# Kernel optimization log

Measured on AMD Instinct MI355X. Metric: run time of the kernel, lower is better.

The kernel has to match this reference:

```python
import jax, jax.numpy as jnp
import numpy as np
import math

B, T, O, D, H, L, FF = 2, 1024, 512, 1024, 16, 4, 4096
MAX_SEQ = 1024


def _ln(x, g, b, eps=1e-5):
    m = jnp.mean(x, -1, keepdims=True)
    v = jnp.mean((x - m) ** 2, -1, keepdims=True)
    return (x - m) * jax.lax.rsqrt(v + eps) * g + b


def _gelu(x):
    return jax.nn.gelu(x, approximate=False)  # torch nn.GELU default = exact erf


def setup_inputs() -> dict:
    key = jax.random.key(0)
    ks = iter(jax.random.split(key, 64))
    std = 0.02
    def w(shape):
        return (jax.random.normal(next(ks), shape, jnp.float32) * std)
    d = {
        'obs': jax.random.normal(next(ks), (B, T, O), jnp.float32),
        # encoder MLP: Linear(O,D), LN, GELU, Linear(D,D), GELU, Linear(D,D), LN
        'enc_w1': w((O, D)), 'enc_b1': jnp.zeros((D,)),
        'enc_g1': jnp.ones((D,)), 'enc_be1': jnp.zeros((D,)),
        'enc_w2': w((D, D)), 'enc_b2': jnp.zeros((D,)),
        'enc_w3': w((D, D)), 'enc_b3': jnp.zeros((D,)),
        'enc_g2': jnp.ones((D,)), 'enc_be2': jnp.zeros((D,)),
        'pos_emb': w((MAX_SEQ, D)),
        # stacked per-layer transformer params [L, ...]
        'ln1_g': jnp.ones((L, D)), 'ln1_b': jnp.zeros((L, D)),
        'wq': w((L, D, D)), 'bq': jnp.zeros((L, D)),
        'wk': w((L, D, D)), 'bk': jnp.zeros((L, D)),
        'wv': w((L, D, D)), 'bv': jnp.zeros((L, D)),
        'wo': w((L, D, D)), 'bo': jnp.zeros((L, D)),
        'ln2_g': jnp.ones((L, D)), 'ln2_b': jnp.zeros((L, D)),
        'mlp_w1': w((L, D, FF)), 'mlp_b1': jnp.zeros((L, FF)),
        'mlp_w2': w((L, FF, D)), 'mlp_b2': jnp.zeros((L, D)),
        'lnf_g': jnp.ones((D,)), 'lnf_b': jnp.zeros((D,)),
        'dec_w': w((D, O)), 'dec_b': jnp.zeros((O,)),
    }
    return d


def reference(obs, enc_w1, enc_b1, enc_g1, enc_be1, enc_w2, enc_b2, enc_w3, enc_b3,
              enc_g2, enc_be2, pos_emb, ln1_g, ln1_b, wq, bq, wk, bk, wv, bv, wo, bo,
              ln2_g, ln2_b, mlp_w1, mlp_b1, mlp_w2, mlp_b2, lnf_g, lnf_b, dec_w, dec_b):
    b, t, _ = obs.shape
    dh = D // H
    scale = 1.0 / math.sqrt(dh)
    # embedder MLP
    h = _gelu(_ln(obs @ enc_w1 + enc_b1, enc_g1, enc_be1))
    h = _gelu(h @ enc_w2 + enc_b2)
    h = _ln(h @ enc_w3 + enc_b3, enc_g2, enc_be2)
    x = h + pos_emb[:t]
    # causal mask [t, t]
    mask = jnp.tril(jnp.ones((t, t), bool))

    def block(x, p):
        g1, b1, Wq, Bq, Wk, Bk, Wv, Bv, Wo, Bo, g2, b2, W1, B1, W2, B2 = p
        hn = _ln(x, g1, b1)
        q = (hn @ Wq + Bq).reshape(b, t, H, dh).transpose(0, 2, 1, 3)
        k = (hn @ Wk + Bk).reshape(b, t, H, dh).transpose(0, 2, 1, 3)
        v = (hn @ Wv + Bv).reshape(b, t, H, dh).transpose(0, 2, 1, 3)
        att = jnp.einsum('bhtd,bhsd->bhts', q, k) * scale
        att = jnp.where(mask, att, -jnp.inf)
        att = jax.nn.softmax(att, axis=-1)
        y = jnp.einsum('bhts,bhsd->bhtd', att, v)
        y = y.transpose(0, 2, 1, 3).reshape(b, t, D)
        x = x + y @ Wo + Bo
        hm = _ln(x, g2, b2)
        x = x + _gelu(hm @ W1 + B1) @ W2 + B2
        return x, None

    stacked = (ln1_g, ln1_b, wq, bq, wk, bk, wv, bv, wo, bo,
               ln2_g, ln2_b, mlp_w1, mlp_b1, mlp_w2, mlp_b2)
    x, _ = jax.lax.scan(block, x, stacked)
    x = _ln(x, lnf_g, lnf_b)
    out_obs = x @ dec_w + dec_b
    return x, out_obs
```

## Files before the change

### kernel.cpp

```cpp
#include <hip/hip_runtime.h>
#include <utility>

typedef unsigned short u16;
typedef __bf16  bf16x8 __attribute__((ext_vector_type(8)));
typedef float   f32x4  __attribute__((ext_vector_type(4)));
typedef unsigned short u16x4 __attribute__((ext_vector_type(4)));

constexpr int Bc = 2, Tc = 1024, Oc = 512, Dc = 1024, Hc = 16, Lc = 4, FFc = 4096;
constexpr int Mc = Bc * Tc;
constexpr int Sq = 3 * Dc;

__device__ __forceinline__ u16 f2b(float f) {
    unsigned u = __float_as_uint(f);
    u = (u + 0x7fffu + ((u >> 16) & 1u)) >> 16;
    return (u16)u;
}
__device__ __forceinline__ float gelu_f(float x) {
    return 0.5f * x * (1.0f + erff(x * 0.7071067811865476f));
}

typedef const __attribute__((address_space(1))) void* gas_p;
typedef __attribute__((address_space(3))) void* las_p;
__device__ __forceinline__ void gload16(const void* g, void* l) {
    __builtin_amdgcn_global_load_lds((gas_p)g, (las_p)l, 16, 0, 0);
}

__global__ __launch_bounds__(256) void wtrans(const float* __restrict__ in,
                                              u16* __restrict__ out, int R, int C,
                                              long inBatch, long outBatch) {
    __shared__ float t[32][33];
    const float* inp = in + (size_t)blockIdx.z * inBatch;
    u16* outp = out + (size_t)blockIdx.z * outBatch;
    const int tx = threadIdx.x & 31, ty = threadIdx.x >> 5;
    const int br = blockIdx.y * 32, bc = blockIdx.x * 32;
#pragma unroll
    for (int i = 0; i < 32; i += 8)
        t[ty + i][tx] = inp[(size_t)(br + ty + i) * C + bc + tx];
    __syncthreads();
#pragma unroll
    for (int i = 0; i < 32; i += 8)
        outp[(size_t)(bc + ty + i) * R + br + tx] = f2b(t[tx][ty + i]);
}

__global__ __launch_bounds__(256) void cvt_bf(const float* __restrict__ in,
                                              u16* __restrict__ out, int n) {
    int i = blockIdx.x * 256 + threadIdx.x;
    if (i * 4 >= n) return;
    float4 v = ((const float4*)in)[i];
    u16x4 r;
    r[0] = f2b(v.x); r[1] = f2b(v.y); r[2] = f2b(v.z); r[3] = f2b(v.w);
    ((u16x4*)out)[i] = r;
}

__global__ __launch_bounds__(256) void pack_qkv_bias(const float* __restrict__ bq,
    const float* __restrict__ bk, const float* __restrict__ bv, float* __restrict__ out) {
    int i = blockIdx.x * 256 + threadIdx.x;
    int l = i / Sq, j = i % Sq;
    float v = (j < Dc) ? bq[l * Dc + j] : (j < 2 * Dc ? bk[l * Dc + j - Dc] : bv[l * Dc + j - 2 * Dc]);
    out[i] = v;
}

__global__ __launch_bounds__(256) void ln_kernel(
    const float* __restrict__ in, const float* __restrict__ gam,
    const float* __restrict__ bet, const float* __restrict__ pos,
    float* __restrict__ outf, u16* __restrict__ outb, int do_gelu) {
    const int row = blockIdx.x, tid = threadIdx.x;
    const float4 v = ((const float4*)(in + (size_t)row * Dc))[tid];
    float s  = v.x + v.y + v.z + v.w;
    float ss = v.x * v.x + v.y * v.y + v.z * v.z + v.w * v.w;
#pragma unroll
    for (int m = 1; m < 64; m <<= 1) {
        s  += __shfl_xor(s,  m, 64);
        ss += __shfl_xor(ss, m, 64);
    }
    __shared__ float red[8];
    const int w = tid >> 6;
    if ((tid & 63) == 0) { red[w] = s; red[4 + w] = ss; }
    __syncthreads();
    s  = red[0] + red[1] + red[2] + red[3];
    ss = red[4] + red[5] + red[6] + red[7];
    const float mean = s * (1.0f / Dc);
    const float rstd = rsqrtf(ss * (1.0f / Dc) - mean * mean + 1e-5f);
    const float4 gv = ((const float4*)gam)[tid];
    const float4 bv = ((const float4*)bet)[tid];
    float y0 = (v.x - mean) * rstd * gv.x + bv.x;
    float y1 = (v.y - mean) * rstd * gv.y + bv.y;
    float y2 = (v.z - mean) * rstd * gv.z + bv.z;
    float y3 = (v.w - mean) * rstd * gv.w + bv.w;
    if (do_gelu) { y0 = gelu_f(y0); y1 = gelu_f(y1); y2 = gelu_f(y2); y3 = gelu_f(y3); }
    if (pos) {
        const float4 pv = ((const float4*)(pos + (size_t)(row & (Tc - 1)) * Dc))[tid];
        y0 += pv.x; y1 += pv.y; y2 += pv.z; y3 += pv.w;
    }
    if (outf) {
        float4 o; o.x = y0; o.y = y1; o.z = y2; o.w = y3;
        ((float4*)(outf + (size_t)row * Dc))[tid] = o;
    }
    if (outb) {
        u16x4 r; r[0] = f2b(y0); r[1] = f2b(y1); r[2] = f2b(y2); r[3] = f2b(y3);
        ((u16x4*)(outb + (size_t)row * Dc))[tid] = r;
    }
}

__global__ __launch_bounds__(256) void red2_ln(
    const float* __restrict__ p, const float* __restrict__ bias,
    const float* __restrict__ resid, float* __restrict__ xfout,
    const float* __restrict__ gam, const float* __restrict__ bet,
    float* __restrict__ lnoutf, u16* __restrict__ lnoutb) {
    const int row = blockIdx.x, tid = threadIdx.x;
    const f32x4 a  = ((const f32x4*)(p + (size_t)row * Dc))[tid];
    const f32x4 b  = ((const f32x4*)(p + (size_t)Mc * Dc + (size_t)row * Dc))[tid];
    const f32x4 bb = ((const f32x4*)bias)[tid];
    const f32x4 r  = ((const f32x4*)(resid + (size_t)row * Dc))[tid];
    f32x4 v;
#pragma unroll
    for (int j = 0; j < 4; ++j) v[j] = a[j] + b[j] + bb[j] + r[j];
    ((f32x4*)(xfout + (size_t)row * Dc))[tid] = v;
    float s  = v[0] + v[1] + v[2] + v[3];
    float ss = v[0]*v[0] + v[1]*v[1] + v[2]*v[2] + v[3]*v[3];
#pragma unroll
    for (int m = 1; m < 64; m <<= 1) {
        s  += __shfl_xor(s,  m, 64);
        ss += __shfl_xor(ss, m, 64);
    }
    __shared__ float red[8];
    const int w = tid >> 6;
    if ((tid & 63) == 0) { red[w] = s; red[4 + w] = ss; }
    __syncthreads();
    s  = red[0] + red[1] + red[2] + red[3];
    ss = red[4] + red[5] + red[6] + red[7];
    const float mean = s * (1.0f / Dc);
    const float rstd = rsqrtf(ss * (1.0f / Dc) - mean * mean + 1e-5f);
    const f32x4 gv = ((const f32x4*)gam)[tid];
    const f32x4 bv = ((const f32x4*)bet)[tid];
    f32x4 y;
#pragma unroll
    for (int j = 0; j < 4; ++j) y[j] = (v[j] - mean) * rstd * gv[j] + bv[j];
    if (lnoutf) ((f32x4*)(lnoutf + (size_t)row * Dc))[tid] = y;
    u16x4 o;
#pragma unroll
    for (int j = 0; j < 4; ++j) o[j] = f2b(y[j]);
    ((u16x4*)(lnoutb + (size_t)row * Dc))[tid] = o;
}

template<int BM, int BN, int FM, int FN, int WM, int WN, int OCC>
__global__ __launch_bounds__(256, OCC) void gemm_k(
    const u16* __restrict__ A, const u16* __restrict__ Bt,
    const float* __restrict__ bias, const float* resid,
    float* Cf, u16* Cb, u16* vTout, int vcol0,
    int M, int N, int Kst, int Kl, int do_gelu) {
    __shared__ u16 sA[2][BM][64];
    __shared__ u16 sB[2][BN][64];
    constexpr int NA = BM / 32;
    constexpr int NB = BN / 32;
    const int tid = threadIdx.x;
    const int lane = tid & 63, w = tid >> 6;
    const int lr = lane & 15, g = lane >> 4;
    const int wm = w / WN, wn = w % WN;

    A  += (size_t)blockIdx.z * Kl;
    Bt += (size_t)blockIdx.z * Kl;
    Cf += (size_t)blockIdx.z * M * N;

    const int gx = gridDim.x;
    const int nwg = gx * gridDim.y;
    const int orig = blockIdx.y * gx + blockIdx.x;
    const int wgid = (orig & 7) * (nwg >> 3) + (orig >> 3);
    const int s = wgid >> 6, q = wgid & 63;
    const int nsx = gx >> 3;
    const int sy = s / nsx, sx = s - sy * nsx;
    const int by = sy * 8 + (q >> 3), bx = sx * 8 + (q & 7);
    const long m0 = (long)by * BM, n0 = (long)bx * BN;

    const f32x4 fzero = {0.f, 0.f, 0.f, 0.f};
    f32x4 acc[FM][FN];
#pragma unroll
    for (int i = 0; i < FM; ++i)
#pragma unroll
        for (int j = 0; j < FN; ++j) acc[i][j] = fzero;

    const int nt = Kl / 64;
    const int srow = lane >> 3, scc = lane & 7;
    const u16* pa[NA];
    const u16* pb[NB];
#pragma unroll
    for (int r = 0; r < NA; ++r)
        pa[r] = A + (size_t)(m0 + r * 32 + w * 8 + srow) * Kst + ((scc ^ srow) * 8);
#pragma unroll
    for (int r = 0; r < NB; ++r)
        pb[r] = Bt + (size_t)(n0 + r * 32 + w * 8 + srow) * Kst + ((scc ^ srow) * 8);

    auto stage = [&](auto curc, int t) {
        constexpr int cu = decltype(curc)::value;
        if (t < nt) {
#pragma unroll
            for (int r = 0; r < NA; ++r) { gload16(pa[r], &sA[cu][r * 32 + w * 8][0]); pa[r] += 64; }
#pragma unroll
            for (int r = 0; r < NB; ++r) { gload16(pb[r], &sB[cu][r * 32 + w * 8][0]); pb[r] += 64; }
        }
    };
    auto compute = [&](auto curc) {
        constexpr int cu = decltype(curc)::value;
#pragma unroll
        for (int ks = 0; ks < 2; ++ks) {
            bf16x8 fa[FM], fb[FN];
#pragma unroll
            for (int mi = 0; mi < FM; ++mi) {
                int row = wm * (16 * FM) + mi * 16 + lr;
                fa[mi] = *(const bf16x8*)&sA[cu][row][((ks * 4 + g) ^ (row & 7)) * 8];
            }
#pragma unroll
            for (int ni = 0; ni < FN; ++ni) {
                int row = wn * (16 * FN) + ni * 16 + lr;
                fb[ni] = *(const bf16x8*)&sB[cu][row][((ks * 4 + g) ^ (row & 7)) * 8];
            }
#pragma unroll
            for (int mi = 0; mi < FM; ++mi)
#pragma unroll
                for (int ni = 0; ni < FN; ++ni)
                    acc[mi][ni] = __builtin_amdgcn_mfma_f32_16x16x32_bf16(
                        fa[mi], fb[ni], acc[mi][ni], 0, 0, 0);
        }
    };
    auto drain_barrier = [&]() {
        asm volatile("s_waitcnt vmcnt(0)" ::: "memory");
        __builtin_amdgcn_sched_barrier(0);
        __syncthreads();
    };

    std::integral_constant<int, 0> c0;
    std::integral_constant<int, 1> c1;
    stage(c0, 0);
    drain_barrier();
    for (int t = 0; t < nt; t += 2) {
        stage(c1, t + 1);
        compute(c0);
        drain_barrier();
        stage(c0, t + 2);
        compute(c1);
        drain_barrier();
    }
#pragma unroll
    for (int mi = 0; mi < FM; ++mi) {
#pragma unroll
        for (int ni = 0; ni < FN; ++ni) {
            const long nc = n0 + wn * (16 * FN) + ni * 16 + lr;
            const float bvv = bias ? bias[nc] : 0.0f;
#pragma unroll
            for (int j = 0; j < 4; ++j) {
                const long mr = m0 + wm * (16 * FM) + mi * 16 + g * 4 + j;
                float v = acc[mi][ni][j] + bvv;
                if (resid) v += resid[(size_t)mr * N + nc];
                if (do_gelu) v = gelu_f(v);
                if (vTout && nc >= vcol0) {
                    const long d = nc - vcol0, t = mr & (Tc - 1), bb = mr >> 10;
                    vTout[((size_t)bb * Dc + d) * Tc + t] = f2b(v);
                } else {
                    if (Cf) Cf[(size_t)mr * N + nc] = v;
                    if (Cb) Cb[(size_t)mr * N + nc] = f2b(v);
                }
            }
        }
    }
}

__global__ __launch_bounds__(256, 2) void attn_kernel(
    const u16* __restrict__ qkv, const u16* __restrict__ Vt, u16* __restrict__ Yg) {
    __shared__ u16 sK[2][64][64];
    __shared__ u16 sV[2][64][64];
    __shared__ u16 sP[4][16][64];
    const int tid = threadIdx.x, w = tid >> 6, lane = tid & 63;
    const int lr = lane & 15, g = lane >> 4;
    const int hw = blockIdx.x;
    const int xcd = hw & 7, slot = hw >> 3;
    const int bh = xcd + 8 * (slot >> 4);
    const int qc = 15 - (slot & 15);
    const int h = bh & 15, b = bh >> 4;
    const int tq0 = qc * 64 + w * 16;
    const u16* Qp = qkv + (size_t)b * Tc * Sq + h * 64;
    const u16* Kp = qkv + (size_t)b * Tc * Sq + Dc + h * 64;
    const u16* Vp = Vt + ((size_t)b * Dc + h * 64) * Tc;

    bf16x8 qf[2];
#pragma unroll
    for (int ks = 0; ks < 2; ++ks)
        qf[ks] = *(const bf16x8*)(Qp + (size_t)(tq0 + lr) * Sq + ks * 32 + g * 8);

    const f32x4 fzero = {0.f, 0.f, 0.f, 0.f};
    f32x4 o[4];
    float mst[4], lst[4];
#pragma unroll
    for (int j = 0; j < 4; ++j) { mst[j] = -1e30f; lst[j] = 0.f; }
#pragma unroll
    for (int ni = 0; ni < 4; ++ni) o[ni] = fzero;

    const int c0 = tid, c1 = tid + 256;
    const int row0 = c0 >> 3, cc0 = c0 & 7;
    const int row1 = c1 >> 3, cc1 = c1 & 7;
    bf16x8 kr[2], vr[2];
    auto kvload = [&](int jk) {
        kr[0] = *(const bf16x8*)(Kp + (size_t)(jk * 64 + row0) * Sq + cc0 * 8);
        kr[1] = *(const bf16x8*)(Kp + (size_t)(jk * 64 + row1) * Sq + cc1 * 8);
        vr[0] = *(const bf16x8*)(Vp + (size_t)row0 * Tc + jk * 64 + cc0 * 8);
        vr[1] = *(const bf16x8*)(Vp + (size_t)row1 * Tc + jk * 64 + cc1 * 8);
    };
    auto kvwrite = [&](int buf) {
        *(bf16x8*)&sK[buf][row0][(cc0 ^ (row0 & 7)) * 8] = kr[0];
        *(bf16x8*)&sK[buf][row1][(cc1 ^ (row1 & 7)) * 8] = kr[1];
        *(bf16x8*)&sV[buf][row0][(cc0 ^ (row0 & 7)) * 8] = vr[0];
        *(bf16x8*)&sV[buf][row1][(cc1 ^ (row1 & 7)) * 8] = vr[1];
    };

    kvload(0);
    kvwrite(0);
    __syncthreads();
    for (int jk = 0; jk <= qc; ++jk) {
        const int cur = jk & 1;
        if (jk < qc) kvload(jk + 1);
        f32x4 s[4];
#pragma unroll
        for (int ni = 0; ni < 4; ++ni) {
            const int row = ni * 16 + lr;
            bf16x8 kf0 = *(const bf16x8*)&sK[cur][row][((0 + g) ^ (lr & 7)) * 8];
            bf16x8 kf1 = *(const bf16x8*)&sK[cur][row][((4 + g) ^ (lr & 7)) * 8];
            s[ni] = __builtin_amdgcn_mfma_f32_16x16x32_bf16(qf[0], kf0, fzero, 0, 0, 0);
            s[ni] = __builtin_amdgcn_mfma_f32_16x16x32_bf16(qf[1], kf1, s[ni], 0, 0, 0);
        }
#pragma unroll
        for (int ni = 0; ni < 4; ++ni)
#pragma unroll
            for (int j = 0; j < 4; ++j) {
                float v = s[ni][j] * 0.125f;
                int tk = jk * 64 + ni * 16 + lr;
                int tq = tq0 + g * 4 + j;
                if (tk > tq) v = -1e30f;
                s[ni][j] = v;
            }
        float fs[4];
#pragma unroll
        for (int j = 0; j < 4; ++j) {
            float pm = fmaxf(fmaxf(s[0][j], s[1][j]), fmaxf(s[2][j], s[3][j]));
            pm = fmaxf(pm, __shfl_xor(pm, 1, 16));
            pm = fmaxf(pm, __shfl_xor(pm, 2, 16));
            pm = fmaxf(pm, __shfl_xor(pm, 4, 16));
            pm = fmaxf(pm, __shfl_xor(pm, 8, 16));
            const float m2 = fmaxf(mst[j], pm);
            fs[j] = __expf(mst[j] - m2);
#pragma unroll
            for (int ni = 0; ni < 4; ++ni)
                s[ni][j] = __expf(s[ni][j] - m2);
            float rsum = s[0][j] + s[1][j] + s[2][j] + s[3][j];
            rsum += __shfl_xor(rsum, 1, 16);
            rsum += __shfl_xor(rsum, 2, 16);
            rsum += __shfl_xor(rsum, 4, 16);
            rsum += __shfl_xor(rsum, 8, 16);
            lst[j] = lst[j] * fs[j] + rsum;
            mst[j] = m2;
        }
#pragma unroll
        for (int ni = 0; ni < 4; ++ni)
#pragma unroll
            for (int j = 0; j < 4; ++j) o[ni][j] *= fs[j];
#pragma unroll
        for (int ni = 0; ni < 4; ++ni)
#pragma unroll
            for (int j = 0; j < 4; ++j) {
                int row = g * 4 + j;
                int col = ni * 16 + lr;
                sP[w][row][(((col >> 3) ^ (row & 7)) << 3) | (col & 7)] = f2b(s[ni][j]);
            }
#pragma unroll
        for (int ks = 0; ks < 2; ++ks) {
            bf16x8 pf = *(const bf16x8*)&sP[w][lr][((ks * 4 + g) ^ (lr & 7)) * 8];
#pragma unroll
            for (int ni = 0; ni < 4; ++ni) {
                const int row = ni * 16 + lr;
                bf16x8 vf = *(const bf16x8*)&sV[cur][row][((ks * 4 + g) ^ (lr & 7)) * 8];
                o[ni] = __builtin_amdgcn_mfma_f32_16x16x32_bf16(pf, vf, o[ni], 0, 0, 0);
            }
        }
        if (jk < qc) kvwrite(cur ^ 1);
        __syncthreads();
    }
#pragma unroll
    for (int ni = 0; ni < 4; ++ni)
#pragma unroll
        for (int j = 0; j < 4; ++j) {
            int tq = tq0 + g * 4 + j;
            int col = h * 64 + ni * 16 + lr;
            Yg[(size_t)(b * Tc + tq) * Dc + col] = f2b(o[ni][j] / lst[j]);
        }
}

extern "C" void kernel_launch(void* const* d_in, const int* in_sizes, int n_in,
                              void* d_out, int out_size, void* d_ws, size_t ws_size,
                              hipStream_t stream) {
    const float* obs    = (const float*)d_in[0];
    const float* enc_w1 = (const float*)d_in[1];
    const float* enc_b1 = (const float*)d_in[2];
    const float* enc_g1 = (const float*)d_in[3];
    const float* enc_be1= (const float*)d_in[4];
    const float* enc_w2 = (const float*)d_in[5];
    const float* enc_b2 = (const float*)d_in[6];
    const float* enc_w3 = (const float*)d_in[7];
    const float* enc_b3 = (const float*)d_in[8];
    const float* enc_g2 = (const float*)d_in[9];
    const float* enc_be2= (const float*)d_in[10];
    const float* pos_emb= (const float*)d_in[11];
    const float* ln1_g  = (const float*)d_in[12];
    const float* ln1_b  = (const float*)d_in[13];
    const float* wq     = (const float*)d_in[14];
    const float* bq     = (const float*)d_in[15];
    const float* wk     = (const float*)d_in[16];
    const float* bk     = (const float*)d_in[17];
    const float* wv     = (const float*)d_in[18];
    const float* bv     = (const float*)d_in[19];
    const float* wo     = (const float*)d_in[20];
    const float* bo     = (const float*)d_in[21];
    const float* ln2_g  = (const float*)d_in[22];
    const float* ln2_b  = (const float*)d_in[23];
    const float* mlp_w1 = (const float*)d_in[24];
    const float* mlp_b1 = (const float*)d_in[25];
    const float* mlp_w2 = (const float*)d_in[26];
    const float* mlp_b2 = (const float*)d_in[27];
    const float* lnf_g  = (const float*)d_in[28];
    const float* lnf_b  = (const float*)d_in[29];
    const float* dec_w  = (const float*)d_in[30];
    const float* dec_b  = (const float*)d_in[31];

    float* out_x = (float*)d_out;
    float* out_o = out_x + (size_t)Mc * Dc;

    char* base = (char*)d_ws;
    size_t off = 0;
    auto ab = [&](size_t e) -> u16* {
        u16* r = (u16*)(base + off); off += (e * 2 + 255) & ~(size_t)255; return r; };
    auto af = [&](size_t e) -> float* {
        float* r = (float*)(base + off); off += (e * 4 + 255) & ~(size_t)255; return r; };

    u16* wt_e1   = ab((size_t)Dc * Oc);
    u16* wt_e2   = ab((size_t)Dc * Dc);
    u16* wt_e3   = ab((size_t)Dc * Dc);
    u16* wtqkv   = ab((size_t)Lc * 3 * Dc * Dc);
    u16* wto     = ab((size_t)Lc * Dc * Dc);
    u16* wtm1    = ab((size_t)Lc * Dc * FFc);
    u16* wtm2    = ab((size_t)Lc * FFc * Dc);
    u16* wt_d    = ab((size_t)Oc * Dc);
    float* qkvb  = af((size_t)Lc * Sq);

    u16*   obs_bf = ab((size_t)Mc * Oc);
    float* tmpf   = af((size_t)Mc * Dc);
    float* xf     = af((size_t)Mc * Dc);
    float* x2f    = af((size_t)Mc * Dc);
    u16*   hn_bf  = ab((size_t)Mc * Dc);
    u16*   qkv    = ab((size_t)Mc * Sq);
    u16*   vT     = ab((size_t)Mc * Dc);
    u16*   y_bf   = ab((size_t)Mc * Dc);
    u16*   ff_bf  = ab((size_t)Mc * FFc);
    float* pk     = af((size_t)2 * Mc * Dc);

    wtrans<<<dim3(Dc / 32, Oc / 32, 1), 256, 0, stream>>>(enc_w1, wt_e1, Oc, Dc, 0, 0);
    wtrans<<<dim3(Dc / 32, Dc / 32, 1), 256, 0, stream>>>(enc_w2, wt_e2, Dc, Dc, 0, 0);
    wtrans<<<dim3(Dc / 32, Dc / 32, 1), 256, 0, stream>>>(enc_w3, wt_e3, Dc, Dc, 0, 0);
    wtrans<<<dim3(Dc / 32, Dc / 32, Lc), 256, 0, stream>>>(wq, wtqkv,            Dc, Dc, (long)Dc * Dc, (long)3 * Dc * Dc);
    wtrans<<<dim3(Dc / 32, Dc / 32, Lc), 256, 0, stream>>>(wk, wtqkv + Dc * Dc,  Dc, Dc, (long)Dc * Dc, (long)3 * Dc * Dc);
    wtrans<<<dim3(Dc / 32, Dc / 32, Lc), 256, 0, stream>>>(wv, wtqkv + 2 * Dc * Dc, Dc, Dc, (long)Dc * Dc, (long)3 * Dc * Dc);
    wtrans<<<dim3(Dc / 32, Dc / 32, Lc), 256, 0, stream>>>(wo, wto, Dc, Dc, (long)Dc * Dc, (long)Dc * Dc);
    wtrans<<<dim3(FFc / 32, Dc / 32, Lc), 256, 0, stream>>>(mlp_w1, wtm1, Dc, FFc, (long)Dc * FFc, (long)Dc * FFc);
    wtrans<<<dim3(Dc / 32, FFc / 32, Lc), 256, 0, stream>>>(mlp_w2, wtm2, FFc, Dc, (long)Dc * FFc, (long)Dc * FFc);
    wtrans<<<dim3(Oc / 32, Dc / 32, 1), 256, 0, stream>>>(dec_w, wt_d, Dc, Oc, 0, 0);
    pack_qkv_bias<<<dim3(Lc * Sq / 256), 256, 0, stream>>>(bq, bk, bv, qkvb);
    cvt_bf<<<dim3((Mc * Oc / 4 + 255) / 256), 256, 0, stream>>>(obs, obs_bf, Mc * Oc);

    auto g128 = [&](const u16* A, const u16* Bt, const float* bias, const float* resid,
                    float* Cf, u16* Cb, u16* vTout, int vcol0,
                    int M, int N, int K, int gel) {
        gemm_k<128, 128, 4, 4, 2, 2, 2><<<dim3(N / 128, M / 128), 256, 0, stream>>>(
            A, Bt, bias, resid, Cf, Cb, vTout, vcol0, M, N, K, K, gel);
    };
    auto g64 = [&](const u16* A, const u16* Bt, const float* bias, const float* resid,
                   float* Cf, u16* Cb, int M, int N, int K, int gel) {
        gemm_k<64, 64, 2, 2, 2, 2, 4><<<dim3(N / 64, M / 64), 256, 0, stream>>>(
            A, Bt, bias, resid, Cf, Cb, nullptr, 0, M, N, K, K, gel);
    };
    auto lnk = [&](const float* in, const float* gg, const float* bb, const float* pos,
                   float* outf, u16* outb, int gel) {
        ln_kernel<<<dim3(Mc), 256, 0, stream>>>(in, gg, bb, pos, outf, outb, gel);
    };

    g64(obs_bf, wt_e1, enc_b1, nullptr, tmpf, nullptr, Mc, Dc, Oc, 0);
    lnk(tmpf, enc_g1, enc_be1, nullptr, nullptr, hn_bf, 1);
    g64(hn_bf, wt_e2, enc_b2, nullptr, nullptr, y_bf, Mc, Dc, Dc, 1);
    g64(y_bf, wt_e3, enc_b3, nullptr, tmpf, nullptr, Mc, Dc, Dc, 0);
    lnk(tmpf, enc_g2, enc_be2, pos_emb, xf, nullptr, 0);

    lnk(xf, ln1_g, ln1_b, nullptr, nullptr, hn_bf, 0);

    for (int l = 0; l < Lc; ++l) {
        g128(hn_bf, wtqkv + (size_t)l * 3 * Dc * Dc, qkvb + (size_t)l * Sq, nullptr,
             nullptr, qkv, vT, 2 * Dc, Mc, Sq, Dc, 0);
        attn_kernel<<<dim3(Bc * Hc * (Tc / 64)), 256, 0, stream>>>(qkv, vT, y_bf);
        g64(y_bf, wto + (size_t)l * Dc * Dc, bo + (size_t)l * Dc, xf, x2f, nullptr, Mc, Dc, Dc, 0);
        lnk(x2f, ln2_g + (size_t)l * Dc, ln2_b + (size_t)l * Dc, nullptr, nullptr, hn_bf, 0);
        g128(hn_bf, wtm1 + (size_t)l * Dc * FFc, mlp_b1 + (size_t)l * FFc, nullptr,
             nullptr, ff_bf, nullptr, 0, Mc, FFc, Dc, 1);
        gemm_k<64, 64, 2, 2, 2, 2, 4><<<dim3(Dc / 64, Mc / 64, 2), 256, 0, stream>>>(
            ff_bf, wtm2 + (size_t)l * FFc * Dc, nullptr, nullptr, pk, nullptr,
            nullptr, 0, Mc, Dc, FFc, FFc / 2, 0);
        if (l < Lc - 1) {
            red2_ln<<<dim3(Mc), 256, 0, stream>>>(
                pk, mlp_b2 + (size_t)l * Dc, x2f, xf,
                ln1_g + (size_t)(l + 1) * Dc, ln1_b + (size_t)(l + 1) * Dc,
                nullptr, hn_bf);
        } else {
            red2_ln<<<dim3(Mc), 256, 0, stream>>>(
                pk, mlp_b2 + (size_t)l * Dc, x2f, xf,
                lnf_g, lnf_b, out_x, hn_bf);
        }
    }

    g64(hn_bf, wt_d, dec_b, nullptr, out_o, nullptr, Mc, Oc, Dc, 0);
}
```

Before: 802.5 us.

## Use single-buffered 128x64 GEMM for QKV/MLP and separate V transpose kernel

Adds a single-buffered GEMM variant with 128x64 tiles and higher occupancy, and uses it for the QKV projection, the MLP up-projection and the split-K MLP down-projection in place of the double-buffered 128x128 and 64x64 kernels. The scattered transposed-V write in the QKV epilogue is removed and replaced by a separate shared-memory transpose kernel that builds V^T from the QKV buffer. The intent is to trade double-buffer overlap for more resident waves to hide latency, and to make the QKV epilogue stores coalesced. The cost is an extra kernel launch plus an extra pass over V, and the loss of load/compute overlap inside each block.

```diff
diff --git a/kernel.cpp b/kernel.cpp
--- a/kernel.cpp
+++ b/kernel.cpp
@@ -40,6 +40,22 @@
 #pragma unroll
     for (int i = 0; i < 32; i += 8)
         outp[(size_t)(bc + ty + i) * R + br + tx] = f2b(t[tx][ty + i]);
+}
+
+__global__ __launch_bounds__(256) void btrans(const u16* __restrict__ in,
+                                              u16* __restrict__ out, int inStride) {
+    __shared__ u16 t[32][33];
+    const u16* inp = in + (size_t)blockIdx.z * Tc * inStride;
+    u16* outp = out + (size_t)blockIdx.z * Dc * Tc;
+    const int tx = threadIdx.x & 31, ty = threadIdx.x >> 5;
+    const int br = blockIdx.y * 32, bc = blockIdx.x * 32;
+#pragma unroll
+    for (int i = 0; i < 32; i += 8)
+        t[ty + i][tx] = inp[(size_t)(br + ty + i) * inStride + bc + tx];
+    __syncthreads();
+#pragma unroll
+    for (int i = 0; i < 32; i += 8)
+        outp[(size_t)(bc + ty + i) * Tc + br + tx] = t[tx][ty + i];
 }
 
 __global__ __launch_bounds__(256) void cvt_bf(const float* __restrict__ in,
@@ -143,12 +159,112 @@
     ((u16x4*)(lnoutb + (size_t)row * Dc))[tid] = o;
 }
 
+__device__ __forceinline__ void xcd_map(int& bx, int& by) {
+    const int gx = gridDim.x;
+    const int nwg = gx * gridDim.y;
+    const int orig = blockIdx.y * gx + blockIdx.x;
+    const int wgid = (orig & 7) * (nwg >> 3) + (orig >> 3);
+    const int s = wgid >> 6, q = wgid & 63;
+    const int nsx = gx >> 3;
+    const int sy = s / nsx, sx = s - sy * nsx;
+    by = sy * 8 + (q >> 3);
+    bx = sx * 8 + (q & 7);
+}
+
+template<int BM, int BN, int FM, int FN, int WM, int WN, int OCC>
+__global__ __launch_bounds__(256, OCC) void gemm_s(
+    const u16* __restrict__ A, const u16* __restrict__ Bt,
+    const float* __restrict__ bias, const float* resid,
+    float* Cf, u16* Cb, int M, int N, int Kst, int Kl, int do_gelu) {
+    __shared__ u16 sA[BM][64];
+    __shared__ u16 sB[BN][64];
+    constexpr int NA = BM / 32;
+    constexpr int NB = BN / 32;
+    const int tid = threadIdx.x;
+    const int lane = tid & 63, w = tid >> 6;
+    const int lr = lane & 15, g = lane >> 4;
+    const int wm = w / WN, wn = w % WN;
+
+    A  += (size_t)blockIdx.z * Kl;
+    Bt += (size_t)blockIdx.z * Kl;
+    Cf += (size_t)blockIdx.z * M * N;
+
+    int bx, by;
+    xcd_map(bx, by);
+    const long m0 = (long)by * BM, n0 = (long)bx * BN;
+
+    const f32x4 fzero = {0.f, 0.f, 0.f, 0.f};
+    f32x4 acc[FM][FN];
+#pragma unroll
+    for (int i = 0; i < FM; ++i)
+#pragma unroll
+        for (int j = 0; j < FN; ++j) acc[i][j] = fzero;
+
+    const int nt = Kl / 64;
+    const int srow = lane >> 3, scc = lane & 7;
+    const u16* pa[NA];
+    const u16* pb[NB];
+#pragma unroll
+    for (int r = 0; r < NA; ++r)
+        pa[r] = A + (size_t)(m0 + r * 32 + w * 8 + srow) * Kst + ((scc ^ srow) * 8);
+#pragma unroll
+    for (int r = 0; r < NB; ++r)
+        pb[r] = Bt + (size_t)(n0 + r * 32 + w * 8 + srow) * Kst + ((scc ^ srow) * 8);
+
+    for (int t = 0; t < nt; ++t) {
+#pragma unroll
+        for (int r = 0; r < NA; ++r) { gload16(pa[r], &sA[r * 32 + w * 8][0]); pa[r] += 64; }
+#pragma unroll
+        for (int r = 0; r < NB; ++r) { gload16(pb[r], &sB[r * 32 + w * 8][0]); pb[r] += 64; }
+        asm volatile("s_waitcnt vmcnt(0)" ::: "memory");
+        __builtin_amdgcn_sched_barrier(0);
+        __syncthreads();
+#pragma unroll
+        for (int ks = 0; ks < 2; ++ks) {
+            bf16x8 fa[FM], fb[FN];
+#pragma unroll
+            for (int mi = 0; mi < FM; ++mi) {
+                int row = wm * (16 * FM) + mi * 16 + lr;
+                fa[mi] = *(const bf16x8*)&sA[row][((ks * 4 + g) ^ (row & 7)) * 8];
+            }
+#pragma unroll
+            for (int ni = 0; ni < FN; ++ni) {
+                int row = wn * (16 * FN) + ni * 16 + lr;
+                fb[ni] = *(const bf16x8*)&sB[row][((ks * 4 + g) ^ (row & 7)) * 8];
+            }
+#pragma unroll
+            for (int mi = 0; mi < FM; ++mi)
+#pragma unroll
+                for (int ni = 0; ni < FN; ++ni)
+                    acc[mi][ni] = __builtin_amdgcn_mfma_f32_16x16x32_bf16(
+                        fa[mi], fb[ni], acc[mi][ni], 0, 0, 0);
+        }
+        __syncthreads();
+    }
+#pragma unroll
+    for (int mi = 0; mi < FM; ++mi) {
+#pragma unroll
+        for (int ni = 0; ni < FN; ++ni) {
+            const long nc = n0 + wn * (16 * FN) + ni * 16 + lr;
+            const float bvv = bias ? bias[nc] : 0.0f;
+#pragma unroll
+            for (int j = 0; j < 4; ++j) {
+                const long mr = m0 + wm * (16 * FM) + mi * 16 + g * 4 + j;
+                float v = acc[mi][ni][j] + bvv;
+                if (resid) v += resid[(size_t)mr * N + nc];
+                if (do_gelu) v = gelu_f(v);
+                if (Cf) Cf[(size_t)mr * N + nc] = v;
+                if (Cb) Cb[(size_t)mr * N + nc] = f2b(v);
+            }
+        }
+    }
+}
+
 template<int BM, int BN, int FM, int FN, int WM, int WN, int OCC>
 __global__ __launch_bounds__(256, OCC) void gemm_k(
     const u16* __restrict__ A, const u16* __restrict__ Bt,
     const float* __restrict__ bias, const float* resid,
-    float* Cf, u16* Cb, u16* vTout, int vcol0,
-    int M, int N, int Kst, int Kl, int do_gelu) {
+    float* Cf, u16* Cb, int M, int N, int Kst, int Kl, int do_gelu) {
     __shared__ u16 sA[2][BM][64];
     __shared__ u16 sB[2][BN][64];
     constexpr int NA = BM / 32;
@@ -162,14 +278,8 @@
     Bt += (size_t)blockIdx.z * Kl;
     Cf += (size_t)blockIdx.z * M * N;
 
-    const int gx = gridDim.x;
-    const int nwg = gx * gridDim.y;
-    const int orig = blockIdx.y * gx + blockIdx.x;
-    const int wgid = (orig & 7) * (nwg >> 3) + (orig >> 3);
-    const int s = wgid >> 6, q = wgid & 63;
-    const int nsx = gx >> 3;
-    const int sy = s / nsx, sx = s - sy * nsx;
-    const int by = sy * 8 + (q >> 3), bx = sx * 8 + (q & 7);
+    int bx, by;
+    xcd_map(bx, by);
     const long m0 = (long)by * BM, n0 = (long)bx * BN;
 
     const f32x4 fzero = {0.f, 0.f, 0.f, 0.f};
@@ -252,13 +362,8 @@
                 float v = acc[mi][ni][j] + bvv;
                 if (resid) v += resid[(size_t)mr * N + nc];
                 if (do_gelu) v = gelu_f(v);
-                if (vTout && nc >= vcol0) {
-                    const long d = nc - vcol0, t = mr & (Tc - 1), bb = mr >> 10;
-                    vTout[((size_t)bb * Dc + d) * Tc + t] = f2b(v);
-                } else {
-                    if (Cf) Cf[(size_t)mr * N + nc] = v;
-                    if (Cb) Cb[(size_t)mr * N + nc] = f2b(v);
-                }
+                if (Cf) Cf[(size_t)mr * N + nc] = v;
+                if (Cb) Cb[(size_t)mr * N + nc] = f2b(v);
             }
         }
     }
@@ -472,16 +577,15 @@
     pack_qkv_bias<<<dim3(Lc * Sq / 256), 256, 0, stream>>>(bq, bk, bv, qkvb);
     cvt_bf<<<dim3((Mc * Oc / 4 + 255) / 256), 256, 0, stream>>>(obs, obs_bf, Mc * Oc);
 
-    auto g128 = [&](const u16* A, const u16* Bt, const float* bias, const float* resid,
-                    float* Cf, u16* Cb, u16* vTout, int vcol0,
-                    int M, int N, int K, int gel) {
-        gemm_k<128, 128, 4, 4, 2, 2, 2><<<dim3(N / 128, M / 128), 256, 0, stream>>>(
-            A, Bt, bias, resid, Cf, Cb, vTout, vcol0, M, N, K, K, gel);
+    auto gS = [&](const u16* A, const u16* Bt, const float* bias, const float* resid,
+                  float* Cf, u16* Cb, int M, int N, int K, int gel) {
+        gemm_s<128, 64, 4, 2, 2, 2, 4><<<dim3(N / 64, M / 128), 256, 0, stream>>>(
+            A, Bt, bias, resid, Cf, Cb, M, N, K, K, gel);
     };
     auto g64 = [&](const u16* A, const u16* Bt, const float* bias, const float* resid,
                    float* Cf, u16* Cb, int M, int N, int K, int gel) {
         gemm_k<64, 64, 2, 2, 2, 2, 4><<<dim3(N / 64, M / 64), 256, 0, stream>>>(
-            A, Bt, bias, resid, Cf, Cb, nullptr, 0, M, N, K, K, gel);
+            A, Bt, bias, resid, Cf, Cb, M, N, K, K, gel);
     };
     auto lnk = [&](const float* in, const float* gg, const float* bb, const float* pos,
                    float* outf, u16* outb, int gel) {
@@ -497,16 +601,17 @@
     lnk(xf, ln1_g, ln1_b, nullptr, nullptr, hn_bf, 0);
 
     for (int l = 0; l < Lc; ++l) {
-        g128(hn_bf, wtqkv + (size_t)l * 3 * Dc * Dc, qkvb + (size_t)l * Sq, nullptr,
-             nullptr, qkv, vT, 2 * Dc, Mc, Sq, Dc, 0);
+        gS(hn_bf, wtqkv + (size_t)l * 3 * Dc * Dc, qkvb + (size_t)l * Sq, nullptr,
+           nullptr, qkv, Mc, Sq, Dc, 0);
+        btrans<<<dim3(Dc / 32, Tc / 32, Bc), 256, 0, stream>>>(qkv + 2 * Dc, vT, Sq);
         attn_kernel<<<dim3(Bc * Hc * (Tc / 64)), 256, 0, stream>>>(qkv, vT, y_bf);
         g64(y_bf, wto + (size_t)l * Dc * Dc, bo + (size_t)l * Dc, xf, x2f, nullptr, Mc, Dc, Dc, 0);
         lnk(x2f, ln2_g + (size_t)l * Dc, ln2_b + (size_t)l * Dc, nullptr, nullptr, hn_bf, 0);
-        g128(hn_bf, wtm1 + (size_t)l * Dc * FFc, mlp_b1 + (size_t)l * FFc, nullptr,
-             nullptr, ff_bf, nullptr, 0, Mc, FFc, Dc, 1);
-        gemm_k<64, 64, 2, 2, 2, 2, 4><<<dim3(Dc / 64, Mc / 64, 2), 256, 0, stream>>>(
+        gS(hn_bf, wtm1 + (size_t)l * Dc * FFc, mlp_b1 + (size_t)l * FFc, nullptr,
+           nullptr, ff_bf, Mc, FFc, Dc, 1);
+        gemm_s<128, 64, 4, 2, 2, 2, 4><<<dim3(Dc / 64, Mc / 128, 2), 256, 0, stream>>>(
             ff_bf, wtm2 + (size_t)l * FFc * Dc, nullptr, nullptr, pk, nullptr,
-            nullptr, 0, Mc, Dc, FFc, FFc / 2, 0);
+            Mc, Dc, FFc, FFc / 2, 0);
         if (l < Lc - 1) {
             red2_ln<<<dim3(Mc), 256, 0, stream>>>(
                 pk, mlp_b2 + (size_t)l * Dc, x2f, xf,
```

New measurement: 750.0 us. -6.5%, faster.
